# Optimization experiments

Measured on AMD Instinct MI355X. Metric: run time of the kernel, lower is better.

The kernel has to match this reference:

```python
import jax, jax.numpy as jnp
from jax import lax
import numpy as np

SHIFT = 0.0
BN_EPS = 1e-5
THRESHOLD = 0.9
GAMMA = 1.0


def _maxpool2(x):
    # 2x2 max pool, stride 2, NCHW
    return lax.reduce_window(x, -jnp.inf, lax.max, (1, 1, 2, 2), (1, 1, 2, 2), 'VALID')


def _conv(x, w, b):
    y = lax.conv_general_dilated(x, w, (1, 1), 'SAME',
                                 dimension_numbers=('NCHW', 'OIHW', 'NCHW'))
    return y + b[None, :, None, None]


def setup_inputs() -> dict:
    key = jax.random.key(0)
    ks = jax.random.split(key, 12)
    B = 8192
    x = jax.random.normal(ks[0], (B, 1, 28, 28), dtype=jnp.float32)
    conv1_w = jax.random.normal(ks[1], (8, 1, 3, 3), dtype=jnp.float32) * 0.1
    conv1_b = jax.random.normal(ks[2], (8,), dtype=jnp.float32) * 0.1
    conv2_w = jax.random.normal(ks[3], (16, 8, 3, 3), dtype=jnp.float32) * 0.1
    conv2_b = jax.random.normal(ks[4], (16,), dtype=jnp.float32) * 0.1
    fc1_w = jax.random.normal(ks[5], (64, 784), dtype=jnp.float32) * 0.05
    fc1_b = jax.random.normal(ks[6], (64,), dtype=jnp.float32) * 0.05
    fc2_w = jax.random.normal(ks[7], (4, 64), dtype=jnp.float32) * 0.1
    fc2_b = jax.random.normal(ks[8], (4,), dtype=jnp.float32) * 0.1
    bn_gamma = jnp.ones((4,), dtype=jnp.float32)
    bn_beta = jnp.zeros((4,), dtype=jnp.float32)
    return dict(x=x, conv1_w=conv1_w, conv1_b=conv1_b, conv2_w=conv2_w,
                conv2_b=conv2_b, fc1_w=fc1_w, fc1_b=fc1_b, fc2_w=fc2_w,
                fc2_b=fc2_b, bn_gamma=bn_gamma, bn_beta=bn_beta)


def reference(x, conv1_w, conv1_b, conv2_w, conv2_b, fc1_w, fc1_b,
              fc2_w, fc2_b, bn_gamma, bn_beta):
    B = x.shape[0]
    # CNN feature extractor
    h = _maxpool2(jax.nn.relu(_conv(x, conv1_w, conv1_b)))   # [B,8,14,14]
    h = _maxpool2(jax.nn.relu(_conv(h, conv2_w, conv2_b)))   # [B,16,7,7]
    flat = h.reshape(B, -1)                                   # [B,784]
    h = jax.nn.relu(flat @ fc1_w.T + fc1_b)                   # [B,64]
    proj = h @ fc2_w.T + fc2_b                                # [B,4]
    # BatchNorm1d (training mode: batch stats, biased variance)
    mean = jnp.mean(proj, axis=0)
    var = jnp.mean((proj - mean) ** 2, axis=0)
    proj = (proj - mean) * lax.rsqrt(var + BN_EPS) * bn_gamma + bn_beta
    # fidelity adjacency (vectorized O(B^2) pairwise squared cosine overlap)
    pn = proj / (jnp.linalg.norm(proj, axis=1, keepdims=True) + 1e-12)
    fid = (pn @ pn.T) ** 2                                    # [B,B]
    off_diag = 1.0 - jnp.eye(B, dtype=proj.dtype)
    adj = jnp.where(fid >= THRESHOLD, 1.0, 0.0) * off_diag
    adj = lax.stop_gradient(adj)  # built via .item() in torch -> detached
    weighted_proj = adj @ proj                                # [B,4]
    # RBF kernel over the fully-flattened feature matrices (scalar)
    diff = proj - weighted_proj
    k_val = jnp.exp(-GAMMA * jnp.sum(diff * diff))
    # combined.sum(dim=1) == row sums + scalar kernel value
    logits = (jnp.sum(proj, axis=1, keepdims=True)
              + jnp.sum(weighted_proj, axis=1, keepdims=True)
              + k_val)                                        # [B,1]
    probs = jax.nn.sigmoid(logits + SHIFT)
    return jnp.concatenate([probs, 1.0 - probs], axis=-1)     # [B,2]
```

## Files before the change

### kernel.cpp

```cpp
#include <hip/hip_runtime.h>
#include <hip/hip_bf16.h>

#define B_IMG 8192
#define FC_ROWS 8
#define FC_NBLK (B_IMG / FC_ROWS)

#define OFF_SD    64
#define OFF_PROJ  128
#define OFF_PN64  (128 + 262144)
#define OFF_PB32  (OFF_PN64 + 262144)
#define OFF_PN32  (OFF_PB32 + 131072)
#define OFF_WP32  (OFF_PN32 + 131072)
#define OFF_W1T   (OFF_WP32 + 131072)
#define OFF_PSUM  (OFF_W1T + 200704)
#define OFF_FLAT  1310720
#define FLAT64_BYTES (8192UL * 784UL * 8UL)

#define H1_CS   10
#define H1_RP   164

__global__ __launch_bounds__(256) void setup_kernel(
    const float* __restrict__ fc1w, float* __restrict__ w1t,
    float* __restrict__ sd) {
    const int t = threadIdx.x;
    if (blockIdx.x == 0 && t == 0) sd[0] = 0.f;
    for (int i = blockIdx.x * 256 + t; i < 784 * 64; i += 64 * 256) {
        const int o = i & 63, k = i >> 6;
        w1t[(k >> 2) * 256 + o * 4 + (k & 3)] = fc1w[o * 784 + k];
    }
}

template <int BUF>
__device__ __forceinline__ void ldpair(
    double2 (&W)[2][4][2][2], const double* __restrict__ h1s,
    int rowb, int c0, int icp) {
#pragma unroll
    for (int wr = 0; wr < 4; ++wr) {
#pragma unroll
        for (int cc = 0; cc < 2; ++cc) {
            const double* p = h1s + (rowb + wr) * H1_RP + (c0 + cc) * H1_CS + icp * 4;
            W[BUF][wr][cc][0] = *(const double2*)p;
            W[BUF][wr][cc][1] = *(const double2*)(p + 2);
        }
    }
}

template <int PHASE>
__device__ __forceinline__ void conv2_step(
    const double2 (&W)[2][4][2][2], const double (&wgt)[9][4],
    double bias2, int c2, int icp, int pys, int px,
    double* __restrict__ h2s) {
    double s00 = 0, s01 = 0, s10 = 0, s11 = 0;
#pragma unroll
    for (int dy = 0; dy < 2; ++dy)
#pragma unroll
        for (int dx = 0; dx < 2; ++dx)
#pragma unroll
            for (int ky = 0; ky < 3; ++ky)
#pragma unroll
                for (int kx = 0; kx < 3; ++kx) {
                    const int wr = dy + ky, wc = dx + kx;
                    const int buf = (wc < 2) ? PHASE : (1 - PHASE);
                    const int sl = wc & 1;
                    double2 lo = W[buf][wr][sl][0];
                    double2 hi = W[buf][wr][sl][1];
                    double a = (dy == 0) ? ((dx == 0) ? s00 : s01)
                                         : ((dx == 0) ? s10 : s11);
                    a = fma(lo.x, wgt[ky * 3 + kx][0], a);
                    a = fma(lo.y, wgt[ky * 3 + kx][1], a);
                    a = fma(hi.x, wgt[ky * 3 + kx][2], a);
                    a = fma(hi.y, wgt[ky * 3 + kx][3], a);
                    if (dy == 0) { if (dx == 0) s00 = a; else s01 = a; }
                    else         { if (dx == 0) s10 = a; else s11 = a; }
                }
    s00 += __shfl_xor(s00, 16);
    s01 += __shfl_xor(s01, 16);
    s10 += __shfl_xor(s10, 16);
    s11 += __shfl_xor(s11, 16);
    if (icp == 0) {
        double mx = fmax(fmax(s00, s01), fmax(s10, s11));
        h2s[c2 * 49 + pys * 7 + px] = fmax(bias2 + mx, 0.0);
    }
}

template <bool F64OUT>
__global__ __launch_bounds__(256) void conv_fused(
    const float* __restrict__ x,
    const float* __restrict__ w1, const float* __restrict__ b1,
    const float* __restrict__ w2, const float* __restrict__ b2,
    void* __restrict__ flatv) {

    __shared__ __align__(16) float  xs[900];
    __shared__ __align__(16) double h1s[16 * H1_RP];
    __shared__ __align__(16) double h2s[784];

    const int b = blockIdx.x;
    const int t = threadIdx.x;
    const float* xb = x + (size_t)b * 784;

    const int c2 = t & 15, icp = (t >> 4) & 1, pys = t >> 5;
    double wgt[9][4];
#pragma unroll
    for (int m = 0; m < 4; ++m) {
        const float* wsrc = w2 + c2 * 72 + (icp * 4 + m) * 9;
#pragma unroll
        for (int j = 0; j < 9; ++j) wgt[j][m] = (double)wsrc[j];
    }
    const double bias2 = (double)b2[c2];

    for (int i = t; i < 900; i += 256) xs[i] = 0.f;
    for (int i = t; i < 480; i += 256) {
        const int cell = i >> 3, ic = i & 7;
        int r, c;
        if (cell < 16)      { r = 0;  c = cell; }
        else if (cell < 32) { r = 15; c = cell - 16; }
        else if (cell < 46) { r = cell - 31; c = 0; }
        else                { r = cell - 45; c = 15; }
        h1s[r * H1_RP + c * H1_CS + ic] = 0.0;
    }
    __syncthreads();
    for (int i = t; i < 784; i += 256) {
        const int yy = i / 28, xx = i - yy * 28;
        xs[(yy + 1) * 30 + (xx + 1)] = xb[i];
    }
    __syncthreads();

    {
        const int c1 = t & 7;
        const int lq = t >> 3;
        double wc[9];
#pragma unroll
        for (int j = 0; j < 9; ++j) wc[j] = (double)w1[c1 * 9 + j];
        const double bb = (double)b1[c1];
#pragma unroll
        for (int it = 0; it < 4; ++it) {
            const int pp = lq + 32 * it;
            if (pp >= 98) break;
            const int py = pp / 7, pxp = pp - py * 7;
            const int px0 = 2 * pxp;
            const float* xbase = &xs[(2 * py) * 30 + 2 * px0];
            double dwin[4][6];
#pragma unroll
            for (int rr = 0; rr < 4; ++rr)
#pragma unroll
                for (int cp = 0; cp < 3; ++cp) {
                    float2 v = *(const float2*)&xbase[rr * 30 + 2 * cp];
                    dwin[rr][2 * cp]     = (double)v.x;
                    dwin[rr][2 * cp + 1] = (double)v.y;
                }
            double s0[2][2] = {{bb, bb}, {bb, bb}};
            double s1[2][2] = {{bb, bb}, {bb, bb}};
#pragma unroll
            for (int dy = 0; dy < 2; ++dy)
#pragma unroll
                for (int dx = 0; dx < 2; ++dx)
#pragma unroll
                    for (int ky = 0; ky < 3; ++ky)
#pragma unroll
                        for (int kx = 0; kx < 3; ++kx) {
                            const double wv = wc[ky * 3 + kx];
                            s0[dy][dx] = fma(dwin[dy + ky][dx + kx],     wv, s0[dy][dx]);
                            s1[dy][dx] = fma(dwin[dy + ky][2 + dx + kx], wv, s1[dy][dx]);
                        }
            double mx0 = fmax(fmax(s0[0][0], s0[0][1]), fmax(s0[1][0], s0[1][1]));
            double mx1 = fmax(fmax(s1[0][0], s1[0][1]), fmax(s1[1][0], s1[1][1]));
            mx0 = fmax(mx0, 0.0);
            mx1 = fmax(mx1, 0.0);
            h1s[(py + 1) * H1_RP + (px0 + 1) * H1_CS + c1] = mx0;
            h1s[(py + 1) * H1_RP + (px0 + 2) * H1_CS + c1] = mx1;
        }
    }
    __syncthreads();

    if (pys < 7) {
        const int rowb = 2 * pys;
        double2 W[2][4][2][2];
        ldpair<0>(W, h1s, rowb, 0, icp);
        ldpair<1>(W, h1s, rowb, 2, icp);
#pragma unroll
        for (int px = 0; px < 7; ++px) {
            if ((px & 1) == 0) {
                conv2_step<0>(W, wgt, bias2, c2, icp, pys, px, h2s);
                if (px < 6) ldpair<0>(W, h1s, rowb, 2 * px + 4, icp);
            } else {
                conv2_step<1>(W, wgt, bias2, c2, icp, pys, px, h2s);
                if (px < 6) ldpair<1>(W, h1s, rowb, 2 * px + 4, icp);
            }
        }
    }
    __syncthreads();

    if (F64OUT) {
        double2* dst = (double2*)((double*)flatv + (size_t)b * 784);
        const double2* src = (const double2*)h2s;
        for (int i = t; i < 392; i += 256) dst[i] = src[i];
    } else {
        float* dst = (float*)flatv + (size_t)b * 784;
        for (int i = t; i < 784; i += 256) dst[i] = (float)h2s[i];
    }
}

template <bool F64IN>
__global__ __launch_bounds__(256) void fc_kernel(
    const void* __restrict__ flatv, const float* __restrict__ w1t,
    const float* __restrict__ fc1b,
    const float* __restrict__ fc2w, const float* __restrict__ fc2b,
    double* __restrict__ proj, double* __restrict__ psum) {

    __shared__ __align__(16) double rows[FC_ROWS][784];
    __shared__ __align__(16) double Hs[FC_ROWS][64];
    __shared__ double w2t[256];

    const int t = threadIdx.x;
    const int row0 = blockIdx.x * FC_ROWS;

    w2t[t] = (double)fc2w[(t & 3) * 64 + (t >> 2)];
    if (F64IN) {
        const double2* src = (const double2*)((const double*)flatv + (size_t)row0 * 784);
        double2* dst = (double2*)&rows[0][0];
        for (int i = t; i < FC_ROWS * 784 / 2; i += 256) dst[i] = src[i];
    } else {
        const float4* src = (const float4*)((const float*)flatv + (size_t)row0 * 784);
        double* dst = &rows[0][0];
        for (int i = t; i < FC_ROWS * 784 / 4; i += 256) {
            float4 f = src[i];
            dst[4 * i + 0] = (double)f.x; dst[4 * i + 1] = (double)f.y;
            dst[4 * i + 2] = (double)f.z; dst[4 * i + 3] = (double)f.w;
        }
    }
    __syncthreads();

    const int o = t & 63, s2 = (t >> 6) * 2;
    const double* rp0 = rows[s2];
    const double* rp1 = rows[s2 + 1];
    const float4* wv4 = (const float4*)w1t;
    double a00 = 0.0, a01 = 0.0, a10 = 0.0, a11 = 0.0;
    for (int k = 0; k < 784; k += 4) {
        double2 p0a = *(const double2*)&rp0[k];
        double2 p0b = *(const double2*)&rp0[k + 2];
        double2 p1a = *(const double2*)&rp1[k];
        double2 p1b = *(const double2*)&rp1[k + 2];
        const float4 wv = wv4[(k >> 2) * 64 + o];
        const double wa = (double)wv.x, wb = (double)wv.y;
        const double wc = (double)wv.z, wd = (double)wv.w;
        a00 = fma(p0a.x, wa, a00);
        a01 = fma(p0a.y, wb, a01);
        a00 = fma(p0b.x, wc, a00);
        a01 = fma(p0b.y, wd, a01);
        a10 = fma(p1a.x, wa, a10);
        a11 = fma(p1a.y, wb, a11);
        a10 = fma(p1b.x, wc, a10);
        a11 = fma(p1b.y, wd, a11);
    }
    const double b1v = (double)fc1b[o];
    Hs[s2][o]     = fmax((a00 + a01) + b1v, 0.0);
    Hs[s2 + 1][o] = fmax((a10 + a11) + b1v, 0.0);
    __syncthreads();

    if (t < 32) {
        const int r = t >> 2, kc = t & 3;
        double sv = (double)fc2b[kc];
#pragma unroll 8
        for (int c = 0; c < 64; ++c) sv = fma(Hs[r][c], w2t[c * 4 + kc], sv);
        proj[(size_t)(row0 + r) * 4 + kc] = sv;
        double ssum = sv, sq = sv * sv;
        ssum += __shfl_xor(ssum, 4);   sq += __shfl_xor(sq, 4);
        ssum += __shfl_xor(ssum, 8);   sq += __shfl_xor(sq, 8);
        ssum += __shfl_xor(ssum, 16);  sq += __shfl_xor(sq, 16);
        if (t < 4) {
            psum[(size_t)blockIdx.x * 8 + t] = ssum;
            psum[(size_t)blockIdx.x * 8 + 4 + t] = sq;
        }
    }
}

__global__ __launch_bounds__(256) void bn_kernel(
    const double* __restrict__ proj, const double* __restrict__ psum,
    const float* __restrict__ gamma, const float* __restrict__ beta,
    float* __restrict__ pb32, float* __restrict__ pn32,
    double* __restrict__ pn64) {

    __shared__ double red[256];
    __shared__ double stats_s[8];
    const int t = threadIdx.x;
    {
        const int c = t & 7, i0 = t >> 3;
        double v = 0.0;
        for (int i = i0; i < FC_NBLK; i += 32) v += psum[(size_t)i * 8 + c];
        red[t] = v;
    }
    __syncthreads();
    if (t < 8) {
        double sacc = 0.0;
        for (int j = 0; j < 32; ++j) sacc += red[t + 8 * j];
        stats_s[t] = sacc;
    }
    __syncthreads();

    const int i = blockIdx.x * 256 + t;
    double2 p01 = ((const double2*)proj)[2 * i];
    double2 p23 = ((const double2*)proj)[2 * i + 1];
    double pv[4] = {p01.x, p01.y, p23.x, p23.y};
    double o[4];
#pragma unroll
    for (int k = 0; k < 4; ++k) {
        double mean = stats_s[k] * (1.0 / 8192.0);
        double var  = stats_s[4 + k] * (1.0 / 8192.0) - mean * mean;
        double inv  = 1.0 / sqrt(var + 1e-5);
        o[k] = (pv[k] - mean) * inv * (double)gamma[k] + (double)beta[k];
    }
    double nrm = sqrt(o[0] * o[0] + o[1] * o[1] + o[2] * o[2] + o[3] * o[3]);
    double innv = 1.0 / (nrm + 1e-12);
    ((float4*)pb32)[i] = make_float4((float)o[0], (float)o[1], (float)o[2], (float)o[3]);
    double n0 = o[0] * innv, n1 = o[1] * innv, n2 = o[2] * innv, n3 = o[3] * innv;
    ((float4*)pn32)[i] = make_float4((float)n0, (float)n1, (float)n2, (float)n3);
    double2* pd = (double2*)(pn64 + (size_t)i * 4);
    pd[0] = make_double2(n0, n1);
    pd[1] = make_double2(n2, n3);
}

#define CHUNK 1024
__global__ __launch_bounds__(256) void adj_kernel(
    const float* __restrict__ pn32, const float* __restrict__ pb32,
    const double* __restrict__ pn64,
    float* __restrict__ wp32, float* __restrict__ sd) {

    __shared__ __align__(16) float4 pns[CHUNK];
    __shared__ __align__(16) float4 pbs[CHUNK];
    __shared__ float bpart[16];

    const int t = threadIdx.x;
    const int tg = t & 15, g = t >> 4;
    const int rowb = blockIdx.x * 32 + g * 2;

    float4 pni[2];
#pragma unroll
    for (int r = 0; r < 2; ++r) pni[r] = ((const float4*)pn32)[rowb + r];
    float w[2][4] = {};

    for (int base = 0; base < 8192; base += CHUNK) {
        for (int i = t; i < CHUNK; i += 256) {
            pns[i] = ((const float4*)pn32)[base + i];
            pbs[i] = ((const float4*)pb32)[base + i];
        }
        __syncthreads();
        for (int jj = 0; jj < CHUNK / 16; ++jj) {
            const int jl = jj * 16 + tg;
            float4 q = pns[jl];
            float4 pj = pbs[jl];
#pragma unroll
            for (int r = 0; r < 2; ++r) {
                float d = fmaf(pni[r].x, q.x, fmaf(pni[r].y, q.y,
                          fmaf(pni[r].z, q.z, pni[r].w * q.w)));
                float fid = d * d;
                float tdiff = fid - 0.9f;
                bool ok;
                if (fabsf(tdiff) < 2e-4f) {
                    const int j = base + jl;
                    const double2* pr = (const double2*)(pn64 + (size_t)(rowb + r) * 4);
                    const double2* pq = (const double2*)(pn64 + (size_t)j * 4);
                    double2 r0 = pr[0], r1 = pr[1], q0 = pq[0], q1 = pq[1];
                    double dd = fma(r0.x, q0.x, fma(r0.y, q0.y,
                                fma(r1.x, q1.x, r1.y * q1.y)));
                    ok = (dd * dd >= 0.9);
                } else {
                    ok = (tdiff >= 0.f);
                }
                float m = ok ? 1.f : 0.f;
                w[r][0] = fmaf(m, pj.x, w[r][0]);
                w[r][1] = fmaf(m, pj.y, w[r][1]);
                w[r][2] = fmaf(m, pj.z, w[r][2]);
                w[r][3] = fmaf(m, pj.w, w[r][3]);
            }
        }
        __syncthreads();
    }
#pragma unroll
    for (int msk = 1; msk < 16; msk <<= 1)
#pragma unroll
        for (int r = 0; r < 2; ++r) {
            w[r][0] += __shfl_xor(w[r][0], msk);
            w[r][1] += __shfl_xor(w[r][1], msk);
            w[r][2] += __shfl_xor(w[r][2], msk);
            w[r][3] += __shfl_xor(w[r][3], msk);
        }
    if (tg == 0) {
        float ds_ = 0.f;
#pragma unroll
        for (int r = 0; r < 2; ++r) {
            float4 pbv = ((const float4*)pb32)[rowb + r];
            float v0 = w[r][0] - pbv.x, v1 = w[r][1] - pbv.y;
            float v2 = w[r][2] - pbv.z, v3 = w[r][3] - pbv.w;
            ((float4*)wp32)[rowb + r] = make_float4(v0, v1, v2, v3);
            float d0 = pbv.x - v0, d1 = pbv.y - v1;
            float d2 = pbv.z - v2, d3 = pbv.w - v3;
            ds_ += d0 * d0 + d1 * d1 + d2 * d2 + d3 * d3;
        }
        bpart[g] = ds_;
    }
    __syncthreads();
    if (t == 0) {
        float sacc = 0.f;
#pragma unroll
        for (int i = 0; i < 16; ++i) sacc += bpart[i];
        atomicAdd(sd, sacc);
    }
}

__global__ __launch_bounds__(256) void final_kernel(
    const float* __restrict__ pb32, const float* __restrict__ wp32,
    const float* __restrict__ sd, float* __restrict__ out) {

    const int i = blockIdx.x * 256 + threadIdx.x;
    const double kv = exp(-(double)sd[0]);
    float4 p = ((const float4*)pb32)[i];
    float4 w = ((const float4*)wp32)[i];
    double logit = (double)p.x + p.y + p.z + p.w
                 + (double)w.x + w.y + w.z + w.w + kv;
    double pr = 1.0 / (1.0 + exp(-logit));
    *(float2*)&out[2 * i] = make_float2((float)pr, (float)(1.0 - pr));
}

extern "C" void kernel_launch(void* const* d_in, const int* in_sizes, int n_in,
                              void* d_out, int out_size, void* d_ws, size_t ws_size,
                              hipStream_t stream) {
    const float* x     = (const float*)d_in[0];
    const float* c1w   = (const float*)d_in[1];
    const float* c1b   = (const float*)d_in[2];
    const float* c2w   = (const float*)d_in[3];
    const float* c2b   = (const float*)d_in[4];
    const float* fc1w  = (const float*)d_in[5];
    const float* fc1b  = (const float*)d_in[6];
    const float* fc2w  = (const float*)d_in[7];
    const float* fc2b  = (const float*)d_in[8];
    const float* gamma = (const float*)d_in[9];
    const float* beta  = (const float*)d_in[10];
    float* out = (float*)d_out;

    char* ws = (char*)d_ws;
    float*  sd    = (float*)(ws + OFF_SD);
    double* proj  = (double*)(ws + OFF_PROJ);
    double* pn64  = (double*)(ws + OFF_PN64);
    float*  pb32  = (float*)(ws + OFF_PB32);
    float*  pn32  = (float*)(ws + OFF_PN32);
    float*  wp32  = (float*)(ws + OFF_WP32);
    float*  w1t   = (float*)(ws + OFF_W1T);
    double* psum  = (double*)(ws + OFF_PSUM);
    void*   flat  = (void*)(ws + OFF_FLAT);

    const bool f64flat = ws_size >= (size_t)OFF_FLAT + FLAT64_BYTES;

    setup_kernel<<<64, 256, 0, stream>>>(fc1w, w1t, sd);
    if (f64flat) {
        conv_fused<true><<<B_IMG, 256, 0, stream>>>(x, c1w, c1b, c2w, c2b, flat);
        fc_kernel<true><<<FC_NBLK, 256, 0, stream>>>(flat, w1t, fc1b, fc2w, fc2b, proj, psum);
    } else {
        conv_fused<false><<<B_IMG, 256, 0, stream>>>(x, c1w, c1b, c2w, c2b, flat);
        fc_kernel<false><<<FC_NBLK, 256, 0, stream>>>(flat, w1t, fc1b, fc2w, fc2b, proj, psum);
    }
    bn_kernel<<<B_IMG / 256, 256, 0, stream>>>(proj, psum, gamma, beta, pb32, pn32, pn64);
    adj_kernel<<<B_IMG / 32, 256, 0, stream>>>(pn32, pb32, pn64, wp32, sd);
    final_kernel<<<B_IMG / 256, 256, 0, stream>>>(pb32, wp32, sd, out);
}
```

Baseline: 356.3 us.

## Split adjacency columns across blocks, fuse setup into conv, single-block final reduction

New measurement: 320.8 us. 9.9% less time.

```diff
diff --git a/kernel.cpp b/kernel.cpp
--- a/kernel.cpp
+++ b/kernel.cpp
@@ -5,30 +5,18 @@
 #define FC_ROWS 8
 #define FC_NBLK (B_IMG / FC_ROWS)
 
-#define OFF_SD    64
 #define OFF_PROJ  128
+#define OFF_WPP   OFF_PROJ
 #define OFF_PN64  (128 + 262144)
 #define OFF_PB32  (OFF_PN64 + 262144)
 #define OFF_PN32  (OFF_PB32 + 131072)
-#define OFF_WP32  (OFF_PN32 + 131072)
-#define OFF_W1T   (OFF_WP32 + 131072)
+#define OFF_W1T   (OFF_PN32 + 131072)
 #define OFF_PSUM  (OFF_W1T + 200704)
 #define OFF_FLAT  1310720
 #define FLAT64_BYTES (8192UL * 784UL * 8UL)
 
 #define H1_CS   10
 #define H1_RP   164
-
-__global__ __launch_bounds__(256) void setup_kernel(
-    const float* __restrict__ fc1w, float* __restrict__ w1t,
-    float* __restrict__ sd) {
-    const int t = threadIdx.x;
-    if (blockIdx.x == 0 && t == 0) sd[0] = 0.f;
-    for (int i = blockIdx.x * 256 + t; i < 784 * 64; i += 64 * 256) {
-        const int o = i & 63, k = i >> 6;
-        w1t[(k >> 2) * 256 + o * 4 + (k & 3)] = fc1w[o * 784 + k];
-    }
-}
 
 template <int BUF>
 __device__ __forceinline__ void ldpair(
@@ -84,10 +72,11 @@
 }
 
 template <bool F64OUT>
-__global__ __launch_bounds__(256) void conv_fused(
+__global__ __launch_bounds__(256, 2) void conv_fused(
     const float* __restrict__ x,
     const float* __restrict__ w1, const float* __restrict__ b1,
     const float* __restrict__ w2, const float* __restrict__ b2,
+    const float* __restrict__ fc1w, float* __restrict__ w1t,
     void* __restrict__ flatv) {
 
     __shared__ __align__(16) float  xs[900];
@@ -97,6 +86,13 @@
     const int b = blockIdx.x;
     const int t = threadIdx.x;
     const float* xb = x + (size_t)b * 784;
+
+    if (b < 64) {
+        for (int i = b * 256 + t; i < 784 * 64; i += 64 * 256) {
+            const int o = i & 63, k = i >> 6;
+            w1t[(k >> 2) * 256 + o * 4 + (k & 3)] = fc1w[o * 784 + k];
+        }
+    }
 
     const int c2 = t & 15, icp = (t >> 4) & 1, pys = t >> 5;
     double wgt[9][4];
@@ -322,23 +318,23 @@
 #define CHUNK 1024
 __global__ __launch_bounds__(256) void adj_kernel(
     const float* __restrict__ pn32, const float* __restrict__ pb32,
-    const double* __restrict__ pn64,
-    float* __restrict__ wp32, float* __restrict__ sd) {
+    const double* __restrict__ pn64, float* __restrict__ wpp) {
 
     __shared__ __align__(16) float4 pns[CHUNK];
     __shared__ __align__(16) float4 pbs[CHUNK];
-    __shared__ float bpart[16];
 
     const int t = threadIdx.x;
     const int tg = t & 15, g = t >> 4;
-    const int rowb = blockIdx.x * 32 + g * 2;
+    const int rb = blockIdx.x >> 1, jh = blockIdx.x & 1;
+    const int rowb = rb * 32 + g * 2;
+    const int jb0 = jh * 4096;
 
     float4 pni[2];
 #pragma unroll
     for (int r = 0; r < 2; ++r) pni[r] = ((const float4*)pn32)[rowb + r];
     float w[2][4] = {};
 
-    for (int base = 0; base < 8192; base += CHUNK) {
+    for (int base = jb0; base < jb0 + 4096; base += CHUNK) {
         for (int i = t; i < CHUNK; i += 256) {
             pns[i] = ((const float4*)pn32)[base + i];
             pbs[i] = ((const float4*)pb32)[base + i];
@@ -385,40 +381,53 @@
             w[r][3] += __shfl_xor(w[r][3], msk);
         }
     if (tg == 0) {
-        float ds_ = 0.f;
-#pragma unroll
-        for (int r = 0; r < 2; ++r) {
-            float4 pbv = ((const float4*)pb32)[rowb + r];
-            float v0 = w[r][0] - pbv.x, v1 = w[r][1] - pbv.y;
-            float v2 = w[r][2] - pbv.z, v3 = w[r][3] - pbv.w;
-            ((float4*)wp32)[rowb + r] = make_float4(v0, v1, v2, v3);
-            float d0 = pbv.x - v0, d1 = pbv.y - v1;
-            float d2 = pbv.z - v2, d3 = pbv.w - v3;
-            ds_ += d0 * d0 + d1 * d1 + d2 * d2 + d3 * d3;
-        }
-        bpart[g] = ds_;
-    }
+#pragma unroll
+        for (int r = 0; r < 2; ++r)
+            ((float4*)wpp)[jh * 8192 + rowb + r] =
+                make_float4(w[r][0], w[r][1], w[r][2], w[r][3]);
+    }
+}
+
+__global__ __launch_bounds__(1024) void final_kernel(
+    const float* __restrict__ pb32, const float* __restrict__ wpp,
+    float* __restrict__ out) {
+
+    __shared__ double lbase[8192];
+    __shared__ double wsum[16];
+    __shared__ double kv_s;
+
+    const int t = threadIdx.x;
+    double sdl = 0.0;
+    for (int r = t; r < 8192; r += 1024) {
+        float4 a  = ((const float4*)wpp)[r];
+        float4 bq = ((const float4*)wpp)[8192 + r];
+        float4 p  = ((const float4*)pb32)[r];
+        float w0 = a.x + bq.x - p.x;
+        float w1 = a.y + bq.y - p.y;
+        float w2 = a.z + bq.z - p.z;
+        float w3 = a.w + bq.w - p.w;
+        double lb = (double)p.x + p.y + p.z + p.w;
+        lb = lb + w0 + w1 + w2 + w3;
+        lbase[r] = lb;
+        float d0 = p.x - w0, d1 = p.y - w1, d2 = p.z - w2, d3 = p.w - w3;
+        sdl += (double)(d0 * d0 + d1 * d1 + d2 * d2 + d3 * d3);
+    }
+#pragma unroll
+    for (int m = 1; m < 64; m <<= 1) sdl += __shfl_xor(sdl, m);
+    if ((t & 63) == 0) wsum[t >> 6] = sdl;
     __syncthreads();
     if (t == 0) {
-        float sacc = 0.f;
-#pragma unroll
-        for (int i = 0; i < 16; ++i) sacc += bpart[i];
-        atomicAdd(sd, sacc);
-    }
-}
-
-__global__ __launch_bounds__(256) void final_kernel(
-    const float* __restrict__ pb32, const float* __restrict__ wp32,
-    const float* __restrict__ sd, float* __restrict__ out) {
-
-    const int i = blockIdx.x * 256 + threadIdx.x;
-    const double kv = exp(-(double)sd[0]);
-    float4 p = ((const float4*)pb32)[i];
-    float4 w = ((const float4*)wp32)[i];
-    double logit = (double)p.x + p.y + p.z + p.w
-                 + (double)w.x + w.y + w.z + w.w + kv;
-    double pr = 1.0 / (1.0 + exp(-logit));
-    *(float2*)&out[2 * i] = make_float2((float)pr, (float)(1.0 - pr));
+        double s = 0.0;
+        for (int i = 0; i < 16; ++i) s += wsum[i];
+        kv_s = exp(-s);
+    }
+    __syncthreads();
+    const double kv = kv_s;
+    for (int r = t; r < 8192; r += 1024) {
+        double logit = lbase[r] + kv;
+        double pr = 1.0 / (1.0 + exp(-logit));
+        *(float2*)&out[2 * r] = make_float2((float)pr, (float)(1.0 - pr));
+    }
 }
 
 extern "C" void kernel_launch(void* const* d_in, const int* in_sizes, int n_in,
@@ -438,27 +447,25 @@
     float* out = (float*)d_out;
 
     char* ws = (char*)d_ws;
-    float*  sd    = (float*)(ws + OFF_SD);
     double* proj  = (double*)(ws + OFF_PROJ);
+    float*  wpp   = (float*)(ws + OFF_WPP);
     double* pn64  = (double*)(ws + OFF_PN64);
     float*  pb32  = (float*)(ws + OFF_PB32);
     float*  pn32  = (float*)(ws + OFF_PN32);
-    float*  wp32  = (float*)(ws + OFF_WP32);
     float*  w1t   = (float*)(ws + OFF_W1T);
     double* psum  = (double*)(ws + OFF_PSUM);
     void*   flat  = (void*)(ws + OFF_FLAT);
 
     const bool f64flat = ws_size >= (size_t)OFF_FLAT + FLAT64_BYTES;
 
-    setup_kernel<<<64, 256, 0, stream>>>(fc1w, w1t, sd);
     if (f64flat) {
-        conv_fused<true><<<B_IMG, 256, 0, stream>>>(x, c1w, c1b, c2w, c2b, flat);
+        conv_fused<true><<<B_IMG, 256, 0, stream>>>(x, c1w, c1b, c2w, c2b, fc1w, w1t, flat);
         fc_kernel<true><<<FC_NBLK, 256, 0, stream>>>(flat, w1t, fc1b, fc2w, fc2b, proj, psum);
     } else {
-        conv_fused<false><<<B_IMG, 256, 0, stream>>>(x, c1w, c1b, c2w, c2b, flat);
+        conv_fused<false><<<B_IMG, 256, 0, stream>>>(x, c1w, c1b, c2w, c2b, fc1w, w1t, flat);
         fc_kernel<false><<<FC_NBLK, 256, 0, stream>>>(flat, w1t, fc1b, fc2w, fc2b, proj, psum);
     }
     bn_kernel<<<B_IMG / 256, 256, 0, stream>>>(proj, psum, gamma, beta, pb32, pn32, pn64);
-    adj_kernel<<<B_IMG / 32, 256, 0, stream>>>(pn32, pb32, pn64, wp32, sd);
-    final_kernel<<<B_IMG / 256, 256, 0, stream>>>(pb32, wp32, sd, out);
-}
+    adj_kernel<<<512, 256, 0, stream>>>(pn32, pb32, pn64, wpp);
+    final_kernel<<<1, 1024, 0, stream>>>(pb32, wpp, out);
+}
```
